# Performance work log

Hardware: AMD Instinct MI355X
Metric: run time of the kernel (lower is better)

The kernel has to match this reference:

```python
import jax, jax.numpy as jnp
import numpy as np

B, V, D, P = 32, 21, 512, 64
IN, OUT = D * P, 720
E, K, R, H = 8, 2, 16, 256
SCALING = 16.0 / R  # lora alpha / rank = 1.0
TEMP = 1.0


def setup_inputs() -> dict:
    key = jax.random.key(0)
    ks = jax.random.split(key, 9)
    s = lambda k, shape, fan: jax.random.normal(k, shape, dtype=jnp.float32) * (1.0 / np.sqrt(fan))
    return {
        "x": jax.random.normal(ks[0], (B, V, D, P), dtype=jnp.float32),
        "W_base": s(ks[1], (OUT, IN), IN),
        "b_base": s(ks[2], (OUT,), IN),
        "W_r1": s(ks[3], (H, D), D),
        "b_r1": s(ks[4], (H,), D),
        "W_r2": s(ks[5], (E, H), H),
        "b_r2": s(ks[6], (E,), H),
        "lora_A": s(ks[7], (E, R, IN), IN),
        "lora_B": s(ks[8], (E, OUT, R), R),
    }


def reference(x, W_base, b_base, W_r1, b_r1, W_r2, b_r2, lora_A, lora_B):
    # base head: flatten last two dims -> linear (dropout is identity in eval)
    flattened = x.reshape(B, V, IN)                      # [B, V, D*P]
    base_out = flattened @ W_base.T + b_base             # [B, V, OUT]

    # learned router on pooled features (dropout identity, no noise in eval)
    pooled = x.mean(axis=(1, 3))                         # [B, D]
    h = jax.nn.gelu(pooled @ W_r1.T + b_r1, approximate=False)
    logits = h @ W_r2.T + b_r2                           # [B, E]
    probs = jax.nn.softmax(logits / TEMP, axis=-1)
    topk_w, topk_idx = jax.lax.top_k(probs, K)           # [B, K]
    topk_w = topk_w / jnp.clip(topk_w.sum(-1, keepdims=True), 1e-6)

    # all LoRA experts on all samples (matches original), then gather top-k
    flat2d = flattened.reshape(B * V, IN)
    low = jnp.einsum('ni,eri->enr', flat2d, lora_A)      # [E, BV, R]
    delta = jnp.einsum('enr,eor->eno', low, lora_B) * SCALING  # [E, BV, OUT]
    stack = delta.reshape(E, B, V, OUT).transpose(1, 0, 2, 3)  # [B, E, V, OUT]
    sel = jnp.take_along_axis(stack, topk_idx[:, :, None, None], axis=1)  # [B, K, V, OUT]
    moe_delta = (topk_w[:, :, None, None] * sel).sum(axis=1)  # [B, V, OUT]

    return base_out + moe_delta, probs
```

## Files before the change

### kernel.cpp

```cpp
#include <hip/hip_runtime.h>
#include <math.h>

constexpr int Bz = 32, Vz = 21, Dz = 512, Pz = 64;
constexpr int INz = Dz * Pz;
constexpr int OUTz = 720;
constexpr int Ez = 8, Rz = 16, Hz = 256;
constexpr int Mz = Bz * Vz;
constexpr int Nz = OUTz + Ez * Rz;
constexpr int Kz = INz;

constexpr int BM = 128, BN = 128, BK = 32;
constexpr int SPLIT = 16;
constexpr int KSL = Kz / SPLIT;
constexpr int NCH = KSL / BK;
constexpr int LDA = 36;

constexpr int BM2 = 256, BN2 = 128, BK2 = 32;
constexpr int SPLIT2 = 16;
constexpr int KSL2 = Kz / SPLIT2;
constexpr int NCH2 = KSL2 / BK2;
constexpr int ABUF = BM2 * BK2;
constexpr int BBUF = BN2 * BK2;
constexpr int SLOT = ABUF + BBUF;

constexpr int CVNB  = 1344;
constexpr int CVCH  = 2048;
constexpr int CVTOT = Mz * (Kz / CVCH);

typedef _Float16 f16x8 __attribute__((ext_vector_type(8)));
typedef __fp16  fp16x2 __attribute__((ext_vector_type(2)));
typedef float f32x4 __attribute__((ext_vector_type(4)));

__device__ __forceinline__ unsigned int cvt2(float a, float b) {
    fp16x2 p = __builtin_amdgcn_cvt_pkrtz(a, b);
    return __builtin_bit_cast(unsigned int, p);
}

__device__ __forceinline__ void barrier_lgkm() {
    asm volatile("s_waitcnt lgkmcnt(0)\n\ts_barrier" ::: "memory");
}

__device__ __forceinline__ void gload16(const _Float16* g, _Float16* l) {
    __builtin_amdgcn_global_load_lds(
        (const __attribute__((address_space(1))) unsigned int*)g,
        (__attribute__((address_space(3))) unsigned int*)l, 16, 0, 0);
}

template <bool PART>
__global__ __launch_bounds__(256, 3)
void gemm_pool_kernel(const float* __restrict__ x, const float* __restrict__ Wb,
                      const float* __restrict__ lA, float* __restrict__ part,
                      float* __restrict__ C, float* __restrict__ pooled)
{
    __shared__ _Float16 As[2][BM * LDA];
    __shared__ _Float16 Bs[2][BN * LDA];
    __shared__ float plocal[BM][NCH / 2];

    const int id = blockIdx.x;
    const int x8 = id & 7;
    const int k8 = id >> 3;
    const int nt = k8 % 7;
    const int mt = (k8 / 7) % 6;
    const int s  = (k8 / 42) * 8 + x8;

    const int t  = threadIdx.x;
    const int r  = t >> 1;
    const int h  = t & 1;
    const int kbase = s * KSL + h * 16;

    int gm = mt * BM + r;
    const bool mval = (gm < Mz);
    if (!mval) gm = Mz - 1;
    const float* pa = x + (size_t)gm * Kz + kbase;

    int gn = nt * BN + r;
    if (gn >= Nz) gn = Nz - 1;
    const float* pb = (gn < OUTz) ? (Wb + (size_t)gn * Kz + kbase)
                                  : (lA + (size_t)(gn - OUTz) * Kz + kbase);

    const int wave = t >> 6, lane = t & 63;
    const int wr = (wave >> 1) * 64;
    const int wc = (wave & 1) * 64;
    const int fl = lane & 15;
    const int ko = (lane >> 4) * 8;

    f32x4 acc[4][4] = {};

    float4 ca[2][4], cb[2][4];
    #pragma unroll
    for (int q = 0; q < 4; ++q) {
        ca[0][q] = *(const float4*)(pa + 4 * q);
        cb[0][q] = *(const float4*)(pb + 4 * q);
        ca[1][q] = *(const float4*)(pa + BK + 4 * q);
        cb[1][q] = *(const float4*)(pb + BK + 4 * q);
    }

    const bool do_pool = (nt == 0) && mval;
    float psum = 0.0f;

#define GSTEP(SET, CIDX)                                                          \
    {                                                                             \
        const int c_ = (CIDX);                                                    \
        if (do_pool) {                                                            \
            psum += (ca[SET][0].x + ca[SET][0].y + ca[SET][0].z + ca[SET][0].w)   \
                  + (ca[SET][1].x + ca[SET][1].y + ca[SET][1].z + ca[SET][1].w)   \
                  + (ca[SET][2].x + ca[SET][2].y + ca[SET][2].z + ca[SET][2].w)   \
                  + (ca[SET][3].x + ca[SET][3].y + ca[SET][3].z + ca[SET][3].w);  \
        }                                                                         \
        if (SET == 1) {                                                           \
            float ps2 = psum + __shfl_down(psum, 1, 64);                          \
            if (do_pool && h == 0) plocal[r][c_ >> 1] = ps2;                      \
            psum = 0.0f;                                                          \
        }                                                                         \
        _Float16* wA = &As[SET][r * LDA + h * 16];                                \
        *((uint4*)wA)     = make_uint4(                                           \
            cvt2(ca[SET][0].x, ca[SET][0].y), cvt2(ca[SET][0].z, ca[SET][0].w),   \
            cvt2(ca[SET][1].x, ca[SET][1].y), cvt2(ca[SET][1].z, ca[SET][1].w));  \
        *((uint4*)wA + 1) = make_uint4(                                           \
            cvt2(ca[SET][2].x, ca[SET][2].y), cvt2(ca[SET][2].z, ca[SET][2].w),   \
            cvt2(ca[SET][3].x, ca[SET][3].y), cvt2(ca[SET][3].z, ca[SET][3].w));  \
        _Float16* wB = &Bs[SET][r * LDA + h * 16];                                \
        *((uint4*)wB)     = make_uint4(                                           \
            cvt2(cb[SET][0].x, cb[SET][0].y), cvt2(cb[SET][0].z, cb[SET][0].w),   \
            cvt2(cb[SET][1].x, cb[SET][1].y), cvt2(cb[SET][1].z, cb[SET][1].w));  \
        *((uint4*)wB + 1) = make_uint4(                                           \
            cvt2(cb[SET][2].x, cb[SET][2].y), cvt2(cb[SET][2].z, cb[SET][2].w),   \
            cvt2(cb[SET][3].x, cb[SET][3].y), cvt2(cb[SET][3].z, cb[SET][3].w));  \
        if (c_ + 2 < NCH) {                                                       \
            const float* qa = pa + (c_ + 2) * BK;                                 \
            const float* qb = pb + (c_ + 2) * BK;                                 \
            _Pragma("unroll")                                                     \
            for (int q = 0; q < 4; ++q) {                                         \
                ca[SET][q] = *(const float4*)(qa + 4 * q);                        \
                cb[SET][q] = *(const float4*)(qb + 4 * q);                        \
            }                                                                     \
        }                                                                         \
        barrier_lgkm();                                                          \
        f16x8 af[4], bfr[4];                                                      \
        _Pragma("unroll")                                                         \
        for (int i = 0; i < 4; ++i)                                               \
            af[i] = *(const f16x8*)(&As[SET][(wr + i * 16 + fl) * LDA + ko]);     \
        _Pragma("unroll")                                                         \
        for (int j = 0; j < 4; ++j)                                               \
            bfr[j] = *(const f16x8*)(&Bs[SET][(wc + j * 16 + fl) * LDA + ko]);    \
        _Pragma("unroll")                                                         \
        for (int i = 0; i < 4; ++i)                                               \
            _Pragma("unroll")                                                     \
            for (int j = 0; j < 4; ++j)                                           \
                acc[i][j] = __builtin_amdgcn_mfma_f32_16x16x32_f16(               \
                                af[i], bfr[j], acc[i][j], 0, 0, 0);               \
    }

    for (int cc = 0; cc < NCH; cc += 2) {
        GSTEP(0, cc)
        GSTEP(1, cc + 1)
    }
#undef GSTEP

    if (nt == 0) {
        __syncthreads();
        for (int idx = t; idx < BM * (NCH / 2); idx += 256) {
            const int rr = idx / (NCH / 2), j = idx % (NCH / 2);
            const int g = mt * BM + rr;
            if (g < Mz) atomicAdd(&pooled[(g / Vz) * Dz + s * (NCH / 2) + j], plocal[rr][j]);
        }
    }

    const int rq = (lane >> 4) * 4;
    float* dst = PART ? (part + (size_t)s * Mz * Nz) : C;
    #pragma unroll
    for (int i = 0; i < 4; ++i) {
        const int gmr0 = mt * BM + wr + i * 16 + rq;
        #pragma unroll
        for (int j = 0; j < 4; ++j) {
            const int gnc = nt * BN + wc + j * 16 + fl;
            if (gnc < Nz) {
                #pragma unroll
                for (int q2 = 0; q2 < 4; ++q2) {
                    const int gmr = gmr0 + q2;
                    if (gmr < Mz) {
                        if (PART) dst[(size_t)gmr * Nz + gnc] = acc[i][j][q2];
                        else      atomicAdd(&dst[(size_t)gmr * Nz + gnc], acc[i][j][q2]);
                    }
                }
            }
        }
    }
}

__global__ __launch_bounds__(256)
void convert_kernel(const float* __restrict__ x, _Float16* __restrict__ xh,
                    float* __restrict__ ppart)
{
    const int t = threadIdx.x;
    for (int g = blockIdx.x; g < CVTOT; g += CVNB) {
        const int row = g >> 4;
        const int kk  = g & 15;
        const int off = kk * CVCH + t * 8;
        const float* src  = x  + (size_t)row * Kz;
        _Float16*    dstp = xh + (size_t)row * Kz;
        const float4 u = *(const float4*)(src + off);
        const float4 v = *(const float4*)(src + off + 4);
        *(uint4*)(dstp + off) = make_uint4(cvt2(u.x, u.y), cvt2(u.z, u.w),
                                           cvt2(v.x, v.y), cvt2(v.z, v.w));
        float sp = (u.x + u.y + u.z + u.w) + (v.x + v.y + v.z + v.w);
        sp += __shfl_xor(sp, 1, 64);
        sp += __shfl_xor(sp, 2, 64);
        sp += __shfl_xor(sp, 4, 64);
        if ((t & 7) == 0)
            ppart[(size_t)row * Dz + kk * 32 + (t >> 3)] = sp;
    }
}

__global__ __launch_bounds__(512, 4)
void gemm_f16_kernel(const _Float16* __restrict__ xh, const float* __restrict__ Wb,
                     const float* __restrict__ lA, float* __restrict__ part)
{
    __shared__ _Float16 sm[3 * SLOT];

    const int id = blockIdx.x;
    const int x8 = id & 7;
    const int k8 = id >> 3;
    const int nt = k8 % 7;
    const int mt = (k8 / 7) % 3;
    const int s  = (k8 / 21) * 8 + x8;

    const int t = threadIdx.x;
    const int wave = t >> 6, lane = t & 63;
    const int rl = lane >> 2, cc = lane & 3;
    const int ccs = cc ^ (rl & 3);

    const size_t kb = (size_t)s * KSL2;

    const int rA0 = (wave)     * 16 + rl;
    const int rA1 = (8 + wave) * 16 + rl;
    const int rB  = wave * 16 + rl;
    const _Float16* gA0 = xh + (size_t)min(mt * BM2 + rA0, Mz - 1) * Kz + kb + ccs * 8;
    const _Float16* gA1 = xh + (size_t)min(mt * BM2 + rA1, Mz - 1) * Kz + kb + ccs * 8;
    const int gn = min(nt * BN2 + rB, Nz - 1);
    const float* gBf = ((gn < OUTz) ? (Wb + (size_t)gn * Kz)
                                    : (lA + (size_t)(gn - OUTz) * Kz)) + kb + ccs * 8;

    const int wr = (wave >> 1) * 64;
    const int wc = (wave & 1) * 64;
    const int fl = lane & 15;
    const int slA = ((lane >> 4) ^ (fl & 3)) * 8;

    float4 bEv[2], bOd[2];

    {
        _Float16* sA = sm;
        gload16(gA0, sA + wave * 512);
        gload16(gA1, sA + (8 + wave) * 512);
        bEv[0] = *(const float4*)(gBf);
        bEv[1] = *(const float4*)(gBf + 4);
    }
    {
        _Float16* sA = sm + SLOT;
        gload16(gA0 + BK2, sA + wave * 512);
        gload16(gA1 + BK2, sA + (8 + wave) * 512);
        bOd[0] = *(const float4*)(gBf + BK2);
        bOd[1] = *(const float4*)(gBf + BK2 + 4);
    }
    asm volatile("s_waitcnt vmcnt(4)" ::: "memory");
    *(uint4*)(sm + ABUF + rB * 32 + cc * 8) = make_uint4(
        cvt2(bEv[0].x, bEv[0].y), cvt2(bEv[0].z, bEv[0].w),
        cvt2(bEv[1].x, bEv[1].y), cvt2(bEv[1].z, bEv[1].w));

    f32x4 acc[4][4] = {};

#define FSTEP(C_, BI, BC)                                                        \
    {                                                                            \
        asm volatile("s_waitcnt lgkmcnt(0)\n\ts_barrier" ::: "memory");          \
        if ((C_) + 2 < NCH2) {                                                   \
            _Float16* sA = sm + (((C_) + 2) % 3) * SLOT;                         \
            const size_t ko_ = (size_t)((C_) + 2) * BK2;                         \
            gload16(gA0 + ko_, sA + wave * 512);                                 \
            gload16(gA1 + ko_, sA + (8 + wave) * 512);                           \
            BI[0] = *(const float4*)(gBf + ko_);                                 \
            BI[1] = *(const float4*)(gBf + ko_ + 4);                             \
        }                                                                        \
        const _Float16* A  = sm + ((C_) % 3) * SLOT;                             \
        const _Float16* Bp = A + ABUF;                                           \
        f16x8 af[4], bfr[4];                                                     \
        _Pragma("unroll")                                                        \
        for (int i = 0; i < 4; ++i)                                              \
            af[i] = *(const f16x8*)(A + (wr + i * 16 + fl) * BK2 + slA);         \
        _Pragma("unroll")                                                        \
        for (int j = 0; j < 4; ++j)                                              \
            bfr[j] = *(const f16x8*)(Bp + (wc + j * 16 + fl) * BK2 + slA);       \
        _Pragma("unroll")                                                        \
        for (int i = 0; i < 4; ++i)                                              \
            _Pragma("unroll")                                                    \
            for (int j = 0; j < 4; ++j)                                          \
                acc[i][j] = __builtin_amdgcn_mfma_f32_16x16x32_f16(              \
                                af[i], bfr[j], acc[i][j], 0, 0, 0);              \
        if ((C_) + 1 < NCH2) {                                                   \
            if ((C_) + 2 < NCH2) asm volatile("s_waitcnt vmcnt(4)" ::: "memory");\
            else                 asm volatile("s_waitcnt vmcnt(0)" ::: "memory");\
            _Float16* sB = sm + (((C_) + 1) % 3) * SLOT + ABUF;                  \
            *(uint4*)(sB + rB * 32 + cc * 8) = make_uint4(                       \
                cvt2(BC[0].x, BC[0].y), cvt2(BC[0].z, BC[0].w),                  \
                cvt2(BC[1].x, BC[1].y), cvt2(BC[1].z, BC[1].w));                 \
        }                                                                        \
    }

    for (int c = 0; c < NCH2; c += 2) {
        FSTEP(c,     bEv, bOd)
        FSTEP(c + 1, bOd, bEv)
    }
#undef FSTEP

    const int rq = (lane >> 4) * 4;
    float* dst = part + (size_t)s * Mz * Nz;
    #pragma unroll
    for (int i = 0; i < 4; ++i) {
        const int gmr0 = mt * BM2 + wr + i * 16 + rq;
        #pragma unroll
        for (int j = 0; j < 4; ++j) {
            const int gnc = nt * BN2 + wc + j * 16 + fl;
            if (gnc < Nz) {
                #pragma unroll
                for (int q2 = 0; q2 < 4; ++q2) {
                    const int gmr = gmr0 + q2;
                    if (gmr < Mz) dst[(size_t)gmr * Nz + gnc] = acc[i][j][q2];
                }
            }
        }
    }
}

template <bool PP>
__global__ __launch_bounds__(256)
void router_kernel(const float* __restrict__ src,
                   const float* __restrict__ Wr1, const float* __restrict__ br1,
                   const float* __restrict__ Wr2, const float* __restrict__ br2,
                   float* __restrict__ probs_out, int* __restrict__ tki, float* __restrict__ tkw)
{
    const int b = blockIdx.x, t = threadIdx.x;
    const int wave = t >> 6, lane = t & 63;
    __shared__ float hbuf[Hz];
    __shared__ float lg[Ez];

    const float sc = 1.0f / (float)(Vz * Pz);
    float pv[8];
    if (PP) {
        float a[8] = {0.f, 0.f, 0.f, 0.f, 0.f, 0.f, 0.f, 0.f};
        #pragma unroll
        for (int v = 0; v < Vz; ++v) {
            const float* pr = src + (size_t)(b * Vz + v) * Dz + lane * 8;
            float4 q0 = *(const float4*)pr;
            float4 q1 = *(const float4*)(pr + 4);
            a[0] += q0.x; a[1] += q0.y; a[2] += q0.z; a[3] += q0.w;
            a[4] += q1.x; a[5] += q1.y; a[6] += q1.z; a[7] += q1.w;
        }
        #pragma unroll
        for (int u = 0; u < 8; ++u) pv[u] = a[u] * sc;
    } else {
        const float* prow = src + b * Dz + lane * 8;
        #pragma unroll
        for (int u = 0; u < 8; ++u) pv[u] = prow[u] * sc;
    }

    for (int i0 = 0; i0 < 64; i0 += 4) {
        float v[4];
        #pragma unroll
        for (int u = 0; u < 4; ++u) {
            const int j = wave * 64 + i0 + u;
            const float* wrow = Wr1 + (size_t)j * Dz + lane * 8;
            float4 w0 = *(const float4*)(wrow);
            float4 w1 = *(const float4*)(wrow + 4);
            v[u] = pv[0]*w0.x + pv[1]*w0.y + pv[2]*w0.z + pv[3]*w0.w
                 + pv[4]*w1.x + pv[5]*w1.y + pv[6]*w1.z + pv[7]*w1.w;
        }
        #pragma unroll
        for (int u = 0; u < 4; ++u) {
            #pragma unroll
            for (int off = 32; off >= 1; off >>= 1) v[u] += __shfl_down(v[u], off, 64);
        }
        if (lane == 0) {
            #pragma unroll
            for (int u = 0; u < 4; ++u) {
                const int j = wave * 64 + i0 + u;
                float a = v[u] + br1[j];
                hbuf[j] = 0.5f * a * (1.0f + erff(a * 0.70710678118654752440f));
            }
        }
    }
    __syncthreads();

    if (t < Ez) {
        const float* w = Wr2 + (size_t)t * Hz;
        float a = br2[t];
        for (int j = 0; j < Hz; ++j) a = fmaf(hbuf[j], w[j], a);
        lg[t] = a;
    }
    __syncthreads();

    if (t == 0) {
        float mx = lg[0];
        for (int e = 1; e < Ez; ++e) mx = fmaxf(mx, lg[e]);
        float p[Ez], ssum = 0.0f;
        for (int e = 0; e < Ez; ++e) { p[e] = expf(lg[e] - mx); ssum += p[e]; }
        const float inv = 1.0f / ssum;
        for (int e = 0; e < Ez; ++e) { p[e] *= inv; probs_out[b * Ez + e] = p[e]; }
        int i0 = 0;
        for (int e = 1; e < Ez; ++e) if (p[e] > p[i0]) i0 = e;
        int i1 = (i0 == 0) ? 1 : 0;
        for (int e = 0; e < Ez; ++e) if (e != i0 && p[e] > p[i1]) i1 = e;
        float s2 = p[i0] + p[i1];
        if (s2 < 1e-6f) s2 = 1e-6f;
        tki[b * 2] = i0; tki[b * 2 + 1] = i1;
        tkw[b * 2] = p[i0] / s2; tkw[b * 2 + 1] = p[i1] / s2;
    }
}

template <bool PART, int SPL>
__global__ __launch_bounds__(256)
void combine_kernel(const float* __restrict__ part, const float* __restrict__ C,
                    const float* __restrict__ bb, const float* __restrict__ loraB,
                    const int* __restrict__ tki, const float* __restrict__ tkw,
                    float* __restrict__ out)
{
    const int m = blockIdx.x;
    const int t = threadIdx.x;
    const int b = m / Vz;
    const int e0 = tki[b * 2], e1 = tki[b * 2 + 1];
    const float w0 = tkw[b * 2], w1 = tkw[b * 2 + 1];

    __shared__ float lw[2 * Rz];
    if (t < 2 * Rz) {
        const int e = (t < Rz) ? e0 : e1;
        const size_t off = (size_t)m * Nz + OUTz + e * Rz + (t & (Rz - 1));
        float v = 0.0f;
        if (PART) {
            #pragma unroll
            for (int ss = 0; ss < SPL; ++ss) v += part[(size_t)ss * Mz * Nz + off];
        } else v = C[off];
        lw[t] = v;
    }
    __syncthreads();

    for (int o = t; o < OUTz; o += 256) {
        float acc = bb[o];
        if (PART) {
            #pragma unroll
            for (int ss = 0; ss < SPL; ++ss)
                acc += part[(size_t)ss * Mz * Nz + (size_t)m * Nz + o];
        } else acc += C[(size_t)m * Nz + o];
        const float* B0 = loraB + ((size_t)e0 * OUTz + o) * Rz;
        const float* B1 = loraB + ((size_t)e1 * OUTz + o) * Rz;
        float d0 = 0.0f, d1 = 0.0f;
        #pragma unroll
        for (int rr = 0; rr < Rz; ++rr) {
            d0 = fmaf(lw[rr], B0[rr], d0);
            d1 = fmaf(lw[Rz + rr], B1[rr], d1);
        }
        out[(size_t)m * OUTz + o] = acc + w0 * d0 + w1 * d1;
    }
}

extern "C" void kernel_launch(void* const* d_in, const int* in_sizes, int n_in,
                              void* d_out, int out_size, void* d_ws, size_t ws_size,
                              hipStream_t stream)
{
    const float* x   = (const float*)d_in[0];
    const float* Wb  = (const float*)d_in[1];
    const float* bb  = (const float*)d_in[2];
    const float* Wr1 = (const float*)d_in[3];
    const float* br1 = (const float*)d_in[4];
    const float* Wr2 = (const float*)d_in[5];
    const float* br2 = (const float*)d_in[6];
    const float* lA  = (const float*)d_in[7];
    const float* lB  = (const float*)d_in[8];
    float* out = (float*)d_out;

    const size_t part2_elems = (size_t)SPLIT2 * Mz * Nz;
    const size_t xh_halves   = (size_t)Mz * Kz;
    const size_t ppart_elems = (size_t)Mz * Dz;
    const size_t need_fast = part2_elems * sizeof(float)
                           + xh_halves * sizeof(_Float16)
                           + ppart_elems * sizeof(float) + 1024;

    const size_t part_elems = (size_t)SPLIT * Mz * Nz;
    const size_t need_old = (part_elems + Bz * Dz + 256) * sizeof(float);

    if (ws_size >= need_fast) {
        float*    part   = (float*)d_ws;
        _Float16* xh     = (_Float16*)(part + part2_elems);
        float*    ppart  = (float*)(xh + xh_halves);
        int*      tki    = (int*)(ppart + ppart_elems);
        float*    tkw    = (float*)(tki + 2 * Bz);

        convert_kernel<<<CVNB, 256, 0, stream>>>(x, xh, ppart);
        gemm_f16_kernel<<<3 * 7 * SPLIT2, 512, 0, stream>>>(xh, Wb, lA, part);
        router_kernel<true><<<Bz, 256, 0, stream>>>(ppart, Wr1, br1, Wr2, br2,
                                                    out + (size_t)Mz * OUTz, tki, tkw);
        combine_kernel<true, SPLIT2><<<Mz, 256, 0, stream>>>(part, nullptr, bb, lB, tki, tkw, out);
    } else if (ws_size >= need_old) {
        float* part   = (float*)d_ws;
        float* pooled = part + part_elems;
        int*   tki    = (int*)(pooled + Bz * Dz);
        float* tkw    = (float*)(tki + 2 * Bz);

        (void)hipMemsetAsync(pooled, 0, Bz * Dz * sizeof(float), stream);

        gemm_pool_kernel<true><<<dim3(7 * 6 * SPLIT), 256, 0, stream>>>(
            x, Wb, lA, part, nullptr, pooled);
        router_kernel<false><<<Bz, 256, 0, stream>>>(pooled, Wr1, br1, Wr2, br2,
                                                     out + (size_t)Mz * OUTz, tki, tkw);
        combine_kernel<true, SPLIT><<<Mz, 256, 0, stream>>>(part, nullptr, bb, lB, tki, tkw, out);
    } else {
        float* C      = (float*)d_ws;
        float* pooled = C + (size_t)Mz * Nz;
        int*   tki    = (int*)(pooled + Bz * Dz);
        float* tkw    = (float*)(tki + 2 * Bz);

        (void)hipMemsetAsync(d_ws, 0, ((size_t)Mz * Nz + Bz * Dz) * sizeof(float), stream);

        gemm_pool_kernel<false><<<dim3(7 * 6 * SPLIT), 256, 0, stream>>>(
            x, Wb, lA, nullptr, C, pooled);
        router_kernel<false><<<Bz, 256, 0, stream>>>(pooled, Wr1, br1, Wr2, br2,
                                                     out + (size_t)Mz * OUTz, tki, tkw);
        combine_kernel<false, SPLIT><<<Mz, 256, 0, stream>>>(nullptr, C, bb, lB, tki, tkw, out);
    }
}
```

Baseline: 333.4 us.

## Enlarge GEMM tile to 256x256 with 1024-thread blocks and padded B smem

Doubles the N tile of the split-K f16 MFMA GEMM to 256 and the block to 16 waves, so each block covers four N tiles instead of seven and re-reads the A (activation) tile from global less often. The B tile in shared memory gets a padded pitch of 40 halves to reduce bank conflicts on the fp32-to-f16 converted weights, and loads are reassigned so each thread handles one A row and one B row per chunk. The cost is far fewer blocks (192 versus 336), so the grid may not fill all CUs. LDS use per block also rises, and the last N tile is mostly padding because N is 848.

```diff
diff --git a/kernel.cpp b/kernel.cpp
--- a/kernel.cpp
+++ b/kernel.cpp
@@ -15,13 +15,14 @@
 constexpr int NCH = KSL / BK;
 constexpr int LDA = 36;
 
-constexpr int BM2 = 256, BN2 = 128, BK2 = 32;
+constexpr int BM2 = 256, BN2 = 256, BK2 = 32;
 constexpr int SPLIT2 = 16;
 constexpr int KSL2 = Kz / SPLIT2;
 constexpr int NCH2 = KSL2 / BK2;
-constexpr int ABUF = BM2 * BK2;
-constexpr int BBUF = BN2 * BK2;
-constexpr int SLOT = ABUF + BBUF;
+constexpr int ASLOT2 = BM2 * BK2;
+constexpr int BPITCH = 40;
+constexpr int BSLOT2 = BN2 * BPITCH;
+constexpr int SLOTH  = ASLOT2 + BSLOT2;
 
 constexpr int CVNB  = 1344;
 constexpr int CVCH  = 2048;
@@ -212,83 +213,75 @@
     }
 }
 
-__global__ __launch_bounds__(512, 4)
+__global__ __launch_bounds__(1024, 4)
 void gemm_f16_kernel(const _Float16* __restrict__ xh, const float* __restrict__ Wb,
                      const float* __restrict__ lA, float* __restrict__ part)
 {
-    __shared__ _Float16 sm[3 * SLOT];
+    __shared__ _Float16 sm[3 * SLOTH];
 
     const int id = blockIdx.x;
     const int x8 = id & 7;
     const int k8 = id >> 3;
-    const int nt = k8 % 7;
-    const int mt = (k8 / 7) % 3;
-    const int s  = (k8 / 21) * 8 + x8;
+    const int nt = k8 & 3;
+    const int mt = (k8 >> 2) % 3;
+    const int s  = (k8 / 12) * 8 + x8;
 
     const int t = threadIdx.x;
     const int wave = t >> 6, lane = t & 63;
-    const int rl = lane >> 2, cc = lane & 3;
-    const int ccs = cc ^ (rl & 3);
+    const int row = t >> 2;
+    const int q4  = t & 3;
+    const int ccs = q4 ^ (row & 3);
+    const int wsl = q4 ^ (row & 3);
 
     const size_t kb = (size_t)s * KSL2;
 
-    const int rA0 = (wave)     * 16 + rl;
-    const int rA1 = (8 + wave) * 16 + rl;
-    const int rB  = wave * 16 + rl;
-    const _Float16* gA0 = xh + (size_t)min(mt * BM2 + rA0, Mz - 1) * Kz + kb + ccs * 8;
-    const _Float16* gA1 = xh + (size_t)min(mt * BM2 + rA1, Mz - 1) * Kz + kb + ccs * 8;
-    const int gn = min(nt * BN2 + rB, Nz - 1);
-    const float* gBf = ((gn < OUTz) ? (Wb + (size_t)gn * Kz)
-                                    : (lA + (size_t)(gn - OUTz) * Kz)) + kb + ccs * 8;
-
-    const int wr = (wave >> 1) * 64;
-    const int wc = (wave & 1) * 64;
+    const int gmA = min(mt * BM2 + row, Mz - 1);
+    const _Float16* gA = xh + (size_t)gmA * Kz + kb + ccs * 8;
+
+    const int gnB = min(nt * BN2 + row, Nz - 1);
+    const float* pb = ((gnB < OUTz) ? (Wb + (size_t)gnB * Kz)
+                                    : (lA + (size_t)(gnB - OUTz) * Kz))
+                      + kb + q4 * 8;
+
+    _Float16* wBb = sm + ASLOT2 + row * BPITCH + wsl * 8;
+
+    const int wr = (wave >> 2) * 64;
+    const int wc = (wave & 3) * 64;
     const int fl = lane & 15;
-    const int slA = ((lane >> 4) ^ (fl & 3)) * 8;
-
-    float4 bEv[2], bOd[2];
-
-    {
-        _Float16* sA = sm;
-        gload16(gA0, sA + wave * 512);
-        gload16(gA1, sA + (8 + wave) * 512);
-        bEv[0] = *(const float4*)(gBf);
-        bEv[1] = *(const float4*)(gBf + 4);
-    }
-    {
-        _Float16* sA = sm + SLOT;
-        gload16(gA0 + BK2, sA + wave * 512);
-        gload16(gA1 + BK2, sA + (8 + wave) * 512);
-        bOd[0] = *(const float4*)(gBf + BK2);
-        bOd[1] = *(const float4*)(gBf + BK2 + 4);
-    }
-    asm volatile("s_waitcnt vmcnt(4)" ::: "memory");
-    *(uint4*)(sm + ABUF + rB * 32 + cc * 8) = make_uint4(
-        cvt2(bEv[0].x, bEv[0].y), cvt2(bEv[0].z, bEv[0].w),
-        cvt2(bEv[1].x, bEv[1].y), cvt2(bEv[1].z, bEv[1].w));
+    const int slx = ((lane >> 4) ^ (fl & 3)) * 8;
+
+    float4 bEv0, bEv1, bOd0, bOd1;
+
+    gload16(gA, sm + wave * 512);
+    bEv0 = *(const float4*)(pb);
+    bEv1 = *(const float4*)(pb + 4);
+    gload16(gA + BK2, sm + SLOTH + wave * 512);
+    bOd0 = *(const float4*)(pb + BK2);
+    bOd1 = *(const float4*)(pb + BK2 + 4);
+    asm volatile("s_waitcnt vmcnt(3)" ::: "memory");
+    *(uint4*)(wBb) = make_uint4(cvt2(bEv0.x, bEv0.y), cvt2(bEv0.z, bEv0.w),
+                                cvt2(bEv1.x, bEv1.y), cvt2(bEv1.z, bEv1.w));
 
     f32x4 acc[4][4] = {};
 
-#define FSTEP(C_, BI, BC)                                                        \
+#define FSTEP(C_, I0, I1, W0, W1)                                                \
     {                                                                            \
         asm volatile("s_waitcnt lgkmcnt(0)\n\ts_barrier" ::: "memory");          \
         if ((C_) + 2 < NCH2) {                                                   \
-            _Float16* sA = sm + (((C_) + 2) % 3) * SLOT;                         \
             const size_t ko_ = (size_t)((C_) + 2) * BK2;                         \
-            gload16(gA0 + ko_, sA + wave * 512);                                 \
-            gload16(gA1 + ko_, sA + (8 + wave) * 512);                           \
-            BI[0] = *(const float4*)(gBf + ko_);                                 \
-            BI[1] = *(const float4*)(gBf + ko_ + 4);                             \
+            gload16(gA + ko_, sm + (((C_) + 2) % 3) * SLOTH + wave * 512);       \
+            I0 = *(const float4*)(pb + ko_);                                     \
+            I1 = *(const float4*)(pb + ko_ + 4);                                 \
         }                                                                        \
-        const _Float16* A  = sm + ((C_) % 3) * SLOT;                             \
-        const _Float16* Bp = A + ABUF;                                           \
+        const _Float16* A  = sm + ((C_) % 3) * SLOTH;                            \
+        const _Float16* Bp = A + ASLOT2;                                         \
         f16x8 af[4], bfr[4];                                                     \
         _Pragma("unroll")                                                        \
         for (int i = 0; i < 4; ++i)                                              \
-            af[i] = *(const f16x8*)(A + (wr + i * 16 + fl) * BK2 + slA);         \
+            af[i] = *(const f16x8*)(A + (wr + i * 16 + fl) * BK2 + slx);         \
         _Pragma("unroll")                                                        \
         for (int j = 0; j < 4; ++j)                                              \
-            bfr[j] = *(const f16x8*)(Bp + (wc + j * 16 + fl) * BK2 + slA);       \
+            bfr[j] = *(const f16x8*)(Bp + (wc + j * 16 + fl) * BPITCH + slx);    \
         _Pragma("unroll")                                                        \
         for (int i = 0; i < 4; ++i)                                              \
             _Pragma("unroll")                                                    \
@@ -296,18 +289,17 @@
                 acc[i][j] = __builtin_amdgcn_mfma_f32_16x16x32_f16(              \
                                 af[i], bfr[j], acc[i][j], 0, 0, 0);              \
         if ((C_) + 1 < NCH2) {                                                   \
-            if ((C_) + 2 < NCH2) asm volatile("s_waitcnt vmcnt(4)" ::: "memory");\
+            if ((C_) + 2 < NCH2) asm volatile("s_waitcnt vmcnt(3)" ::: "memory");\
             else                 asm volatile("s_waitcnt vmcnt(0)" ::: "memory");\
-            _Float16* sB = sm + (((C_) + 1) % 3) * SLOT + ABUF;                  \
-            *(uint4*)(sB + rB * 32 + cc * 8) = make_uint4(                       \
-                cvt2(BC[0].x, BC[0].y), cvt2(BC[0].z, BC[0].w),                  \
-                cvt2(BC[1].x, BC[1].y), cvt2(BC[1].z, BC[1].w));                 \
+            _Float16* dB = wBb + (((C_) + 1) % 3) * SLOTH;                       \
+            *(uint4*)(dB) = make_uint4(cvt2(W0.x, W0.y), cvt2(W0.z, W0.w),       \
+                                       cvt2(W1.x, W1.y), cvt2(W1.z, W1.w));      \
         }                                                                        \
     }
 
     for (int c = 0; c < NCH2; c += 2) {
-        FSTEP(c,     bEv, bOd)
-        FSTEP(c + 1, bOd, bEv)
+        FSTEP(c,     bEv0, bEv1, bOd0, bOd1)
+        FSTEP(c + 1, bOd0, bOd1, bEv0, bEv1)
     }
 #undef FSTEP
 
@@ -493,7 +485,7 @@
         float*    tkw    = (float*)(tki + 2 * Bz);
 
         convert_kernel<<<CVNB, 256, 0, stream>>>(x, xh, ppart);
-        gemm_f16_kernel<<<3 * 7 * SPLIT2, 512, 0, stream>>>(xh, Wb, lA, part);
+        gemm_f16_kernel<<<3 * 4 * SPLIT2, 1024, 0, stream>>>(xh, Wb, lA, part);
         router_kernel<true><<<Bz, 256, 0, stream>>>(ppart, Wr1, br1, Wr2, br2,
                                                     out + (size_t)Mz * OUTz, tki, tkw);
         combine_kernel<true, SPLIT2><<<Mz, 256, 0, stream>>>(part, nullptr, bb, lB, tki, tkw, out);
```

After: 363.4 us. 9.0% more time.
